# Optimization experiments

Measured on AMD Instinct MI355X. Metric: run time of the kernel, lower is better.

Reference implementation:

```python
import jax, jax.numpy as jnp
import numpy as np

NUM_TAGS = 512
START_TAG = 510
STOP_TAG = 511
BATCH = 128
SEQ_LEN = 512
NEG_INF = -10000.0


def setup_inputs() -> dict:
    key = jax.random.key(0)
    k1, k2, k3 = jax.random.split(key, 3)
    inputs = jax.random.normal(k1, (BATCH, SEQ_LEN, NUM_TAGS), dtype=jnp.float32)
    tags = jax.random.randint(k2, (BATCH, SEQ_LEN), 0, NUM_TAGS)
    transitions = jax.random.normal(k3, (NUM_TAGS, NUM_TAGS), dtype=jnp.float32)
    # match the torch __init__ sentinel masking of the transition matrix
    transitions = transitions.at[START_TAG, :].set(NEG_INF)
    transitions = transitions.at[:, STOP_TAG].set(NEG_INF)
    return {"inputs": inputs, "tags": tags, "transitions": transitions}


def reference(inputs, tags, transitions):
    # inputs: [B, S, T] emission scores; transitions[j, i] = score of i -> j
    B, S, T = inputs.shape
    alpha0 = jnp.full((B, T), NEG_INF, dtype=inputs.dtype)
    alpha0 = alpha0.at[:, START_TAG].set(0.0)

    def step(alpha, emit):
        # alpha: [B, T] (prev tags), emit: [B, T] (next tags)
        # scores[b, next, prev] = alpha[b, prev] + transitions[next, prev]
        scores = alpha[:, None, :] + transitions[None, :, :]  # [B, T, T]
        new_alpha = emit + jax.nn.logsumexp(scores, axis=-1)   # [B, T]
        return new_alpha, None

    emits = jnp.moveaxis(inputs, 1, 0)  # [S, B, T]
    alpha, _ = jax.lax.scan(step, alpha0, emits)

    terminal = alpha + transitions[STOP_TAG][None, :]  # [B, T]
    losses = jax.nn.logsumexp(terminal, axis=-1)       # [B]
    return jnp.sum(losses)
```

## Files before the change

### kernel.cpp

```cpp
#include <hip/hip_runtime.h>
#include <stdint.h>

#define NTAGS 512
#define STAG 510
#define PTAG 511
#define SEQ 512
#define L2E 1.4426950408889634f
#define LN2 0.6931471805599453f
#define MARGIN 13

typedef int   v8i __attribute__((ext_vector_type(8)));
typedef float v4f __attribute__((ext_vector_type(4)));

__device__ __forceinline__ float fexp2(float x) {
#if __has_builtin(__builtin_amdgcn_exp2f)
    return __builtin_amdgcn_exp2f(x);
#else
    float r; asm("v_exp_f32 %0, %1\n\ts_nop 1" : "=v"(r) : "v"(x)); return r;
#endif
}

#define DPPMAX(X, CTRL) fmaxf((X), __int_as_float(__builtin_amdgcn_update_dpp( \
    0, __float_as_int(X), (CTRL), 0xF, 0xF, false)))

#define STEP_SYNC() asm volatile("s_waitcnt lgkmcnt(0)\n\ts_barrier" ::: "memory")

#define WS_SC   196608
#define WS_PART 204800

__global__ void crf_setup_k(const float* __restrict__ trans, uint8_t* __restrict__ ws)
{
    int t = blockIdx.x * blockDim.x + threadIdx.x;
    int n = t >> 4, KB = t & 15;
    const float* row = trans + n * NTAGS;
    int wq = KB >> 1, h = KB & 1;
    float v[32]; float mx = -3.0e38f;
    #pragma unroll
    for (int k = 0; k < 32; ++k) {
        int p = wq*64 + (k & 3)*16 + h*8 + (k >> 2);
        v[k] = row[p]; mx = fmaxf(mx, v[k]);
    }
    int e = (int)floorf(mx * L2E - 2.90689059f);
    int byt = e + 127; byt = byt < 0 ? 0 : (byt > 254 ? 254 : byt);
    float eeff = (float)(byt - 127);
    uint32_t out[6] = {0u,0u,0u,0u,0u,0u};
    #pragma unroll
    for (int k = 0; k < 32; ++k) {
        float q = exp2f(v[k] * L2E - eeff);
        int code;
        if      (q < 2.0f) code = (int)(q * 8.0f + 0.5f);
        else if (q < 4.0f) code = 16 + (int)((q - 2.0f) * 4.0f + 0.5f);
        else               code = 24 + (int)((q - 4.0f) * 2.0f + 0.5f);
        code = code > 31 ? 31 : code;
        int bp = 6*k, d = bp >> 5, off = bp & 31;
        out[d] |= (uint32_t)code << off;
        if (off > 26) out[d+1] |= (uint32_t)code >> (32 - off);
    }
    uint32_t* E6 = (uint32_t*)ws;
    int base = (n*16 + KB) * 6;
    #pragma unroll
    for (int d = 0; d < 6; ++d) E6[base + d] = out[d];
    ws[WS_SC + n*16 + (KB & 3)*4 + (KB >> 2)] = (uint8_t)byt;
}

__global__ __launch_bounds__(512, 2) void crf_main_k(
    const float* __restrict__ inp, const float* __restrict__ trans,
    const uint8_t* __restrict__ ws, float* __restrict__ part)
{
    __shared__ uint8_t aqb[2*8192];
    __shared__ int     mxp[2*16];
    __shared__ float   mxb[16*8];
    __shared__ float   ssum[16*8];
    __shared__ float   Gb[16];

    const int tid = threadIdx.x;
    const int w = tid >> 6, l = tid & 63, c = l & 15, g = l >> 4;
    const int wg = blockIdx.x;
    const int b0 = g * 4;
    const int SCA = 0x78787878;

    v8i Bf[16];
    int esc[4];
    #pragma unroll
    for (int i = 0; i < 4; ++i) {
        const int n = (w*4 + i)*16 + c;
        esc[i] = *(const int*)(ws + WS_SC + n*16 + g*4);
        #pragma unroll
        for (int kk = 0; kk < 4; ++kk) {
            const uint2* p2 = (const uint2*)((const uint32_t*)ws + (n*16 + kk*4 + g)*6);
            uint2 d0 = p2[0], d1 = p2[1], d2 = p2[2];
            v8i bv;
            bv[0]=(int)d0.x; bv[1]=(int)d0.y; bv[2]=(int)d1.x;
            bv[3]=(int)d1.y; bv[4]=(int)d2.x; bv[5]=(int)d2.y;
            bv[6]=0; bv[7]=0;
            Bf[i*4 + kk] = bv;
        }
    }
    #pragma unroll
    for (int i = 0; i < 16; ++i) asm volatile("" : "+v"(Bf[i]));
    #pragma unroll
    for (int i = 0; i < 4; ++i)  asm volatile("" : "+v"(esc[i]));

    const float* ep[4];
    #pragma unroll
    for (int j = 0; j < 4; ++j)
        ep[j] = inp + (size_t)(wg*16 + b0 + j) * (SEQ*NTAGS) + w*64 + c;

    int aqoff[4];
    #pragma unroll
    for (int j = 0; j < 4; ++j) {
        int bb = b0 + j;
        aqoff[j] = bb*128 + (((w*4 + (c>>2)) ^ (bb & 7)) << 2) + (c & 3);
    }

    float vv[4][4];
    {
        float tr[4];
        #pragma unroll
        for (int i = 0; i < 4; ++i) tr[i] = trans[(w*64 + i*16 + c)*NTAGS + STAG];
        #pragma unroll
        for (int j = 0; j < 4; ++j) {
            #pragma unroll
            for (int i = 0; i < 4; ++i)
                vv[j][i] = ep[j][i*16] + tr[i];
        }
    }
    float Mj[4];
    #pragma unroll
    for (int j = 0; j < 4; ++j) {
        float m = fmaxf(fmaxf(vv[j][0], vv[j][1]), fmaxf(vv[j][2], vv[j][3]));
        #pragma unroll
        for (int msk = 1; msk <= 8; msk <<= 1) m = fmaxf(m, __shfl_xor(m, msk, 64));
        if (c == 0) mxb[(b0 + j)*8 + w] = m;
    }
    __syncthreads();
    float G[4];
    #pragma unroll
    for (int j = 0; j < 4; ++j) {
        float m = -3.0e38f;
        #pragma unroll
        for (int k = 0; k < 8; ++k) m = fmaxf(m, mxb[(b0 + j)*8 + k]);
        Mj[j] = m;
        G[j] = m * L2E;
    }
    {
        uint32_t* AQ = (uint32_t*)(aqb + 8192);
        #pragma unroll
        for (int j = 0; j < 4; ++j) {
            float q0 = fexp2((vv[j][0] - Mj[j]) * L2E + 7.0f);
            float q1 = fexp2((vv[j][1] - Mj[j]) * L2E + 7.0f);
            float q2 = fexp2((vv[j][2] - Mj[j]) * L2E + 7.0f);
            float q3 = fexp2((vv[j][3] - Mj[j]) * L2E + 7.0f);
            int t_ = __builtin_amdgcn_cvt_pk_fp8_f32(q0, q1, 0, false);
            t_ = __builtin_amdgcn_cvt_pk_fp8_f32(q2, q3, t_, true);
            AQ[aqoff[j]] = (uint32_t)t_;
        }
    }
    if (w == 0 && c == 0) { int4 z; z.x=0; z.y=0; z.z=0; z.w=0; *(int4*)&mxp[16 + g*4] = z; }

    float emn[4][4];
    #pragma unroll
    for (int j = 0; j < 4; ++j) ep[j] += NTAGS;
    #pragma unroll
    for (int j = 0; j < 4; ++j) {
        #pragma unroll
        for (int i = 0; i < 4; ++i) emn[j][i] = ep[j][i*16];
    }
    __syncthreads();

    int aoffA[8];
    #pragma unroll
    for (int kk = 0; kk < 4; ++kk) {
        aoffA[2*kk]   = c*32 + ((kk*8 + g*2)     ^ (c & 7));
        aoffA[2*kk+1] = c*32 + ((kk*8 + g*2 + 1) ^ (c & 7));
    }

#define MFMA_K(KK) do { \
    v8i A_; \
    *(int4*)&A_       = aq4[aoffA[2*(KK)]]; \
    *(((int4*)&A_)+1) = aq4[aoffA[2*(KK)+1]]; \
    D[0] = __builtin_amdgcn_mfma_scale_f32_16x16x128_f8f6f4(A_, Bf[0*4+(KK)], D[0], 0, 2, (KK), SCA, (KK), esc[0]); \
    D[1] = __builtin_amdgcn_mfma_scale_f32_16x16x128_f8f6f4(A_, Bf[1*4+(KK)], D[1], 0, 2, (KK), SCA, (KK), esc[1]); \
    D[2] = __builtin_amdgcn_mfma_scale_f32_16x16x128_f8f6f4(A_, Bf[2*4+(KK)], D[2], 0, 2, (KK), SCA, (KK), esc[2]); \
    D[3] = __builtin_amdgcn_mfma_scale_f32_16x16x128_f8f6f4(A_, Bf[3*4+(KK)], D[3], 0, 2, (KK), SCA, (KK), esc[3]); \
} while (0)

    for (int s = 1; s < SEQ; ++s) {
        const int cur = s & 1, nxt = cur ^ 1;

        int4 Pv = *(const int4*)&mxp[cur*16 + g*4];
        int Rj[4]; float dmj[4];
        #pragma unroll
        for (int j = 0; j < 4; ++j) {
            Rj[j] = ((const int*)&Pv)[j] + MARGIN;
            dmj[j] = (float)(7 - Rj[j]);
        }

        float emx[4][4];
        #pragma unroll
        for (int j = 0; j < 4; ++j) {
            #pragma unroll
            for (int i = 0; i < 4; ++i)
                emx[j][i] = fexp2(fmaf(emn[j][i], L2E, dmj[j]));
        }
        if (s < SEQ - 1) {
            #pragma unroll
            for (int j = 0; j < 4; ++j) ep[j] += NTAGS;
            #pragma unroll
            for (int j = 0; j < 4; ++j) {
                #pragma unroll
                for (int i = 0; i < 4; ++i) emn[j][i] = ep[j][i*16];
            }
        }

        const int4* aq4 = (const int4*)(aqb + cur*8192);

        v4f D[4];
        #pragma unroll
        for (int i = 0; i < 4; ++i) { D[i][0]=0.f; D[i][1]=0.f; D[i][2]=0.f; D[i][3]=0.f; }
        __builtin_amdgcn_s_setprio(1);
        MFMA_K(0); MFMA_K(1); MFMA_K(2); MFMA_K(3);
        __builtin_amdgcn_s_setprio(0);

        if (s < SEQ - 1) {
            #pragma unroll
            for (int j = 0; j < 4; ++j) G[j] += (float)Rj[j];

            float vq[4][4];
            #pragma unroll
            for (int j = 0; j < 4; ++j) {
                #pragma unroll
                for (int i = 0; i < 4; ++i)
                    vq[j][i] = fminf(D[i][j] * emx[j][i], 448.0f);
            }
            uint32_t* AQ = (uint32_t*)(aqb + nxt*8192);
            #pragma unroll
            for (int j = 0; j < 4; ++j) {
                int t_ = __builtin_amdgcn_cvt_pk_fp8_f32(vq[j][0], vq[j][1], 0, false);
                t_ = __builtin_amdgcn_cvt_pk_fp8_f32(vq[j][2], vq[j][3], t_, true);
                AQ[aqoff[j]] = (uint32_t)t_;
            }
            if (w == 0) {
                int4 post;
                #pragma unroll
                for (int j = 0; j < 4; ++j) {
                    float bm = fmaxf(fmaxf(vq[j][0], vq[j][1]), fmaxf(vq[j][2], vq[j][3]));
                    bm = DPPMAX(bm, 0xB1); bm = DPPMAX(bm, 0x4E);
                    bm = DPPMAX(bm, 0x141); bm = DPPMAX(bm, 0x140);
                    int be = (int)((__float_as_uint(bm) >> 23) & 255u) - 127;
                    be = be < -30 ? -30 : be;
                    ((int*)&post)[j] = be - 7;
                }
                if (c == 0) *(int4*)&mxp[nxt*16 + g*4] = post;
            }
            STEP_SYNC();
        } else {
            float ts[4];
            #pragma unroll
            for (int i = 0; i < 4; ++i) ts[i] = trans[PTAG*NTAGS + w*64 + i*16 + c];
            float x[4][4];
            #pragma unroll
            for (int j = 0; j < 4; ++j) {
                #pragma unroll
                for (int i = 0; i < 4; ++i)
                    x[j][i] = __log2f(D[i][j]) + (emn[j][i] + ts[i]) * L2E;
            }
            #pragma unroll
            for (int j = 0; j < 4; ++j) {
                float m = fmaxf(fmaxf(x[j][0], x[j][1]), fmaxf(x[j][2], x[j][3]));
                #pragma unroll
                for (int msk = 1; msk <= 8; msk <<= 1) m = fmaxf(m, __shfl_xor(m, msk, 64));
                if (c == 0) mxb[(b0 + j)*8 + w] = m;
            }
            if (w == 0 && c == 0) {
                #pragma unroll
                for (int j = 0; j < 4; ++j) Gb[b0 + j] = G[j];
            }
            __syncthreads();
            #pragma unroll
            for (int j = 0; j < 4; ++j) {
                float XM = -3.0e38f;
                #pragma unroll
                for (int k = 0; k < 8; ++k) XM = fmaxf(XM, mxb[(b0 + j)*8 + k]);
                float sj = fexp2(x[j][0] - XM) + fexp2(x[j][1] - XM)
                         + fexp2(x[j][2] - XM) + fexp2(x[j][3] - XM);
                #pragma unroll
                for (int msk = 1; msk <= 8; msk <<= 1) sj += __shfl_xor(sj, msk, 64);
                if (c == 0) ssum[(b0 + j)*8 + w] = sj;
            }
            __syncthreads();
            if (tid < 16) {
                float S = 0.f, XM = -3.0e38f;
                #pragma unroll
                for (int k = 0; k < 8; ++k) { S += ssum[tid*8 + k]; XM = fmaxf(XM, mxb[tid*8 + k]); }
                part[wg*16 + tid] = LN2 * (Gb[tid] + XM + __log2f(S));
            }
        }
    }
#undef MFMA_K
}

__global__ void crf_final_k(const float* __restrict__ part, float* __restrict__ out)
{
    int t = threadIdx.x;
    float vsum = part[t] + part[t + 64];
    #pragma unroll
    for (int off = 32; off; off >>= 1) vsum += __shfl_down(vsum, off, 64);
    if (t == 0) out[0] = vsum;
}

extern "C" void kernel_launch(void* const* d_in, const int* in_sizes, int n_in,
                              void* d_out, int out_size, void* d_ws, size_t ws_size,
                              hipStream_t stream)
{
    (void)in_sizes; (void)n_in; (void)out_size; (void)ws_size;
    const float* inp   = (const float*)d_in[0];
    const float* trans = (const float*)d_in[2];
    uint8_t* ws = (uint8_t*)d_ws;
    float* part = (float*)(ws + WS_PART);

    crf_setup_k<<<64, 128, 0, stream>>>(trans, ws);
    crf_main_k<<<8, 512, 0, stream>>>(inp, trans, ws, part);
    crf_final_k<<<1, 64, 0, stream>>>(part, (float*)d_out);
}
```

Measured before the change: 646.4 us.

## Halve waves per block, give each wave twice the tag columns, hoist A loads

After: 851.8 us. 31.8% more time.

```diff
diff --git a/kernel.cpp b/kernel.cpp
--- a/kernel.cpp
+++ b/kernel.cpp
@@ -33,11 +33,10 @@
     int t = blockIdx.x * blockDim.x + threadIdx.x;
     int n = t >> 4, KB = t & 15;
     const float* row = trans + n * NTAGS;
-    int wq = KB >> 1, h = KB & 1;
     float v[32]; float mx = -3.0e38f;
     #pragma unroll
     for (int k = 0; k < 32; ++k) {
-        int p = wq*64 + (k & 3)*16 + h*8 + (k >> 2);
+        int p = (KB>>2)*128 + (((KB>>1)&1)*4 + (k&3))*16 + (KB&1)*8 + (k>>2);
         v[k] = row[p]; mx = fmaxf(mx, v[k]);
     }
     int e = (int)floorf(mx * L2E - 2.90689059f);
@@ -63,14 +62,14 @@
     ws[WS_SC + n*16 + (KB & 3)*4 + (KB >> 2)] = (uint8_t)byt;
 }
 
-__global__ __launch_bounds__(512, 2) void crf_main_k(
+__global__ __launch_bounds__(256, 1) void crf_main_k(
     const float* __restrict__ inp, const float* __restrict__ trans,
     const uint8_t* __restrict__ ws, float* __restrict__ part)
 {
     __shared__ uint8_t aqb[2*8192];
     __shared__ int     mxp[2*16];
-    __shared__ float   mxb[16*8];
-    __shared__ float   ssum[16*8];
+    __shared__ float   mxb[16*4];
+    __shared__ float   ssum[16*4];
     __shared__ float   Gb[16];
 
     const int tid = threadIdx.x;
@@ -79,11 +78,11 @@
     const int b0 = g * 4;
     const int SCA = 0x78787878;
 
-    v8i Bf[16];
-    int esc[4];
-    #pragma unroll
-    for (int i = 0; i < 4; ++i) {
-        const int n = (w*4 + i)*16 + c;
+    v8i Bf[32];
+    int esc[8];
+    #pragma unroll
+    for (int i = 0; i < 8; ++i) {
+        const int n = (w*8 + i)*16 + c;
         esc[i] = *(const int*)(ws + WS_SC + n*16 + g*4);
         #pragma unroll
         for (int kk = 0; kk < 4; ++kk) {
@@ -97,77 +96,22 @@
         }
     }
     #pragma unroll
-    for (int i = 0; i < 16; ++i) asm volatile("" : "+v"(Bf[i]));
-    #pragma unroll
-    for (int i = 0; i < 4; ++i)  asm volatile("" : "+v"(esc[i]));
+    for (int i = 0; i < 32; ++i) asm volatile("" : "+a"(Bf[i]));
+    #pragma unroll
+    for (int i = 0; i < 8; ++i)  asm volatile("" : "+v"(esc[i]));
 
     const float* ep[4];
     #pragma unroll
     for (int j = 0; j < 4; ++j)
-        ep[j] = inp + (size_t)(wg*16 + b0 + j) * (SEQ*NTAGS) + w*64 + c;
-
-    int aqoff[4];
+        ep[j] = inp + (size_t)(wg*16 + b0 + j) * (SEQ*NTAGS) + w*128 + c;
+
+    int aqoff0[4], aqoff1[4];
     #pragma unroll
     for (int j = 0; j < 4; ++j) {
         int bb = b0 + j;
-        aqoff[j] = bb*128 + (((w*4 + (c>>2)) ^ (bb & 7)) << 2) + (c & 3);
-    }
-
-    float vv[4][4];
-    {
-        float tr[4];
-        #pragma unroll
-        for (int i = 0; i < 4; ++i) tr[i] = trans[(w*64 + i*16 + c)*NTAGS + STAG];
-        #pragma unroll
-        for (int j = 0; j < 4; ++j) {
-            #pragma unroll
-            for (int i = 0; i < 4; ++i)
-                vv[j][i] = ep[j][i*16] + tr[i];
-        }
-    }
-    float Mj[4];
-    #pragma unroll
-    for (int j = 0; j < 4; ++j) {
-        float m = fmaxf(fmaxf(vv[j][0], vv[j][1]), fmaxf(vv[j][2], vv[j][3]));
-        #pragma unroll
-        for (int msk = 1; msk <= 8; msk <<= 1) m = fmaxf(m, __shfl_xor(m, msk, 64));
-        if (c == 0) mxb[(b0 + j)*8 + w] = m;
-    }
-    __syncthreads();
-    float G[4];
-    #pragma unroll
-    for (int j = 0; j < 4; ++j) {
-        float m = -3.0e38f;
-        #pragma unroll
-        for (int k = 0; k < 8; ++k) m = fmaxf(m, mxb[(b0 + j)*8 + k]);
-        Mj[j] = m;
-        G[j] = m * L2E;
-    }
-    {
-        uint32_t* AQ = (uint32_t*)(aqb + 8192);
-        #pragma unroll
-        for (int j = 0; j < 4; ++j) {
-            float q0 = fexp2((vv[j][0] - Mj[j]) * L2E + 7.0f);
-            float q1 = fexp2((vv[j][1] - Mj[j]) * L2E + 7.0f);
-            float q2 = fexp2((vv[j][2] - Mj[j]) * L2E + 7.0f);
-            float q3 = fexp2((vv[j][3] - Mj[j]) * L2E + 7.0f);
-            int t_ = __builtin_amdgcn_cvt_pk_fp8_f32(q0, q1, 0, false);
-            t_ = __builtin_amdgcn_cvt_pk_fp8_f32(q2, q3, t_, true);
-            AQ[aqoff[j]] = (uint32_t)t_;
-        }
-    }
-    if (w == 0 && c == 0) { int4 z; z.x=0; z.y=0; z.z=0; z.w=0; *(int4*)&mxp[16 + g*4] = z; }
-
-    float emn[4][4];
-    #pragma unroll
-    for (int j = 0; j < 4; ++j) ep[j] += NTAGS;
-    #pragma unroll
-    for (int j = 0; j < 4; ++j) {
-        #pragma unroll
-        for (int i = 0; i < 4; ++i) emn[j][i] = ep[j][i*16];
-    }
-    __syncthreads();
-
+        aqoff0[j] = bb*128 + (((w*8 + 0 + (c>>2)) ^ (bb & 7)) << 2) + (c & 3);
+        aqoff1[j] = bb*128 + (((w*8 + 4 + (c>>2)) ^ (bb & 7)) << 2) + (c & 3);
+    }
     int aoffA[8];
     #pragma unroll
     for (int kk = 0; kk < 4; ++kk) {
@@ -175,32 +119,94 @@
         aoffA[2*kk+1] = c*32 + ((kk*8 + g*2 + 1) ^ (c & 7));
     }
 
+    float vv[4][8];
+    {
+        float tr[8];
+        #pragma unroll
+        for (int i = 0; i < 8; ++i) tr[i] = trans[(w*128 + i*16 + c)*NTAGS + STAG];
+        #pragma unroll
+        for (int j = 0; j < 4; ++j) {
+            #pragma unroll
+            for (int i = 0; i < 8; ++i)
+                vv[j][i] = ep[j][i*16] + tr[i];
+        }
+    }
+    float Mj[4];
+    #pragma unroll
+    for (int j = 0; j < 4; ++j) {
+        float m = -3.0e38f;
+        #pragma unroll
+        for (int i = 0; i < 8; ++i) m = fmaxf(m, vv[j][i]);
+        #pragma unroll
+        for (int msk = 1; msk <= 8; msk <<= 1) m = fmaxf(m, __shfl_xor(m, msk, 64));
+        if (c == 0) mxb[(b0 + j)*4 + w] = m;
+    }
+    __syncthreads();
+    float G[4];
+    #pragma unroll
+    for (int j = 0; j < 4; ++j) {
+        float m = -3.0e38f;
+        #pragma unroll
+        for (int k = 0; k < 4; ++k) m = fmaxf(m, mxb[(b0 + j)*4 + k]);
+        Mj[j] = m;
+        G[j] = m * L2E;
+    }
+    {
+        uint32_t* AQ = (uint32_t*)(aqb + 8192);
+        #pragma unroll
+        for (int j = 0; j < 4; ++j) {
+            float q[8];
+            #pragma unroll
+            for (int i = 0; i < 8; ++i) q[i] = fexp2((vv[j][i] - Mj[j]) * L2E + 7.0f);
+            int t0 = __builtin_amdgcn_cvt_pk_fp8_f32(q[0], q[1], 0, false);
+            t0 = __builtin_amdgcn_cvt_pk_fp8_f32(q[2], q[3], t0, true);
+            int t1 = __builtin_amdgcn_cvt_pk_fp8_f32(q[4], q[5], 0, false);
+            t1 = __builtin_amdgcn_cvt_pk_fp8_f32(q[6], q[7], t1, true);
+            AQ[aqoff0[j]] = (uint32_t)t0;
+            AQ[aqoff1[j]] = (uint32_t)t1;
+        }
+    }
+    if (w == 0 && c == 0) { int4 z; z.x=0; z.y=0; z.z=0; z.w=0; *(int4*)&mxp[16 + g*4] = z; }
+
+    float emn[4][8];
+    #pragma unroll
+    for (int j = 0; j < 4; ++j) ep[j] += NTAGS;
+    #pragma unroll
+    for (int j = 0; j < 4; ++j) {
+        #pragma unroll
+        for (int i = 0; i < 8; ++i) emn[j][i] = ep[j][i*16];
+    }
+    __syncthreads();
+
 #define MFMA_K(KK) do { \
     v8i A_; \
-    *(int4*)&A_       = aq4[aoffA[2*(KK)]]; \
-    *(((int4*)&A_)+1) = aq4[aoffA[2*(KK)+1]]; \
-    D[0] = __builtin_amdgcn_mfma_scale_f32_16x16x128_f8f6f4(A_, Bf[0*4+(KK)], D[0], 0, 2, (KK), SCA, (KK), esc[0]); \
-    D[1] = __builtin_amdgcn_mfma_scale_f32_16x16x128_f8f6f4(A_, Bf[1*4+(KK)], D[1], 0, 2, (KK), SCA, (KK), esc[1]); \
-    D[2] = __builtin_amdgcn_mfma_scale_f32_16x16x128_f8f6f4(A_, Bf[2*4+(KK)], D[2], 0, 2, (KK), SCA, (KK), esc[2]); \
-    D[3] = __builtin_amdgcn_mfma_scale_f32_16x16x128_f8f6f4(A_, Bf[3*4+(KK)], D[3], 0, 2, (KK), SCA, (KK), esc[3]); \
+    *(int4*)&A_       = Areg[2*(KK)]; \
+    *(((int4*)&A_)+1) = Areg[2*(KK)+1]; \
+    _Pragma("unroll") \
+    for (int i = 0; i < 8; ++i) \
+        D[i] = __builtin_amdgcn_mfma_scale_f32_16x16x128_f8f6f4(A_, Bf[i*4+(KK)], D[i], 0, 2, (KK), SCA, (KK), esc[i]); \
 } while (0)
 
     for (int s = 1; s < SEQ; ++s) {
         const int cur = s & 1, nxt = cur ^ 1;
 
         int4 Pv = *(const int4*)&mxp[cur*16 + g*4];
+        const int4* aq4 = (const int4*)(aqb + cur*8192);
+        int4 Areg[8];
+        #pragma unroll
+        for (int t = 0; t < 8; ++t) Areg[t] = aq4[aoffA[t]];
+
         int Rj[4]; float dmj[4];
         #pragma unroll
         for (int j = 0; j < 4; ++j) {
             Rj[j] = ((const int*)&Pv)[j] + MARGIN;
             dmj[j] = (float)(7 - Rj[j]);
         }
-
-        float emx[4][4];
+        float emx[4][8];
         #pragma unroll
         for (int j = 0; j < 4; ++j) {
             #pragma unroll
-            for (int i = 0; i < 4; ++i)
+            for (int i = 0; i < 8; ++i)
                 emx[j][i] = fexp2(fmaf(emn[j][i], L2E, dmj[j]));
         }
         if (s < SEQ - 1) {
@@ -209,15 +215,13 @@
             #pragma unroll
             for (int j = 0; j < 4; ++j) {
                 #pragma unroll
-                for (int i = 0; i < 4; ++i) emn[j][i] = ep[j][i*16];
-            }
-        }
-
-        const int4* aq4 = (const int4*)(aqb + cur*8192);
-
-        v4f D[4];
-        #pragma unroll
-        for (int i = 0; i < 4; ++i) { D[i][0]=0.f; D[i][1]=0.f; D[i][2]=0.f; D[i][3]=0.f; }
+                for (int i = 0; i < 8; ++i) emn[j][i] = ep[j][i*16];
+            }
+        }
+
+        v4f D[8];
+        #pragma unroll
+        for (int i = 0; i < 8; ++i) { D[i][0]=0.f; D[i][1]=0.f; D[i][2]=0.f; D[i][3]=0.f; }
         __builtin_amdgcn_s_setprio(1);
         MFMA_K(0); MFMA_K(1); MFMA_K(2); MFMA_K(3);
         __builtin_amdgcn_s_setprio(0);
@@ -226,25 +230,30 @@
             #pragma unroll
             for (int j = 0; j < 4; ++j) G[j] += (float)Rj[j];
 
-            float vq[4][4];
-            #pragma unroll
-            for (int j = 0; j < 4; ++j) {
-                #pragma unroll
-                for (int i = 0; i < 4; ++i)
+            float vq[4][8];
+            #pragma unroll
+            for (int j = 0; j < 4; ++j) {
+                #pragma unroll
+                for (int i = 0; i < 8; ++i)
                     vq[j][i] = fminf(D[i][j] * emx[j][i], 448.0f);
             }
             uint32_t* AQ = (uint32_t*)(aqb + nxt*8192);
             #pragma unroll
             for (int j = 0; j < 4; ++j) {
-                int t_ = __builtin_amdgcn_cvt_pk_fp8_f32(vq[j][0], vq[j][1], 0, false);
-                t_ = __builtin_amdgcn_cvt_pk_fp8_f32(vq[j][2], vq[j][3], t_, true);
-                AQ[aqoff[j]] = (uint32_t)t_;
+                int t0 = __builtin_amdgcn_cvt_pk_fp8_f32(vq[j][0], vq[j][1], 0, false);
+                t0 = __builtin_amdgcn_cvt_pk_fp8_f32(vq[j][2], vq[j][3], t0, true);
+                int t1 = __builtin_amdgcn_cvt_pk_fp8_f32(vq[j][4], vq[j][5], 0, false);
+                t1 = __builtin_amdgcn_cvt_pk_fp8_f32(vq[j][6], vq[j][7], t1, true);
+                AQ[aqoff0[j]] = (uint32_t)t0;
+                AQ[aqoff1[j]] = (uint32_t)t1;
             }
             if (w == 0) {
                 int4 post;
                 #pragma unroll
                 for (int j = 0; j < 4; ++j) {
-                    float bm = fmaxf(fmaxf(vq[j][0], vq[j][1]), fmaxf(vq[j][2], vq[j][3]));
+                    float bm = -3.0e38f;
+                    #pragma unroll
+                    for (int i = 0; i < 8; ++i) bm = fmaxf(bm, vq[j][i]);
                     bm = DPPMAX(bm, 0xB1); bm = DPPMAX(bm, 0x4E);
                     bm = DPPMAX(bm, 0x141); bm = DPPMAX(bm, 0x140);
                     int be = (int)((__float_as_uint(bm) >> 23) & 255u) - 127;
@@ -255,22 +264,24 @@
             }
             STEP_SYNC();
         } else {
-            float ts[4];
-            #pragma unroll
-            for (int i = 0; i < 4; ++i) ts[i] = trans[PTAG*NTAGS + w*64 + i*16 + c];
-            float x[4][4];
-            #pragma unroll
-            for (int j = 0; j < 4; ++j) {
-                #pragma unroll
-                for (int i = 0; i < 4; ++i)
+            float ts[8];
+            #pragma unroll
+            for (int i = 0; i < 8; ++i) ts[i] = trans[PTAG*NTAGS + w*128 + i*16 + c];
+            float x[4][8];
+            #pragma unroll
+            for (int j = 0; j < 4; ++j) {
+                #pragma unroll
+                for (int i = 0; i < 8; ++i)
                     x[j][i] = __log2f(D[i][j]) + (emn[j][i] + ts[i]) * L2E;
             }
             #pragma unroll
             for (int j = 0; j < 4; ++j) {
-                float m = fmaxf(fmaxf(x[j][0], x[j][1]), fmaxf(x[j][2], x[j][3]));
+                float m = -3.0e38f;
+                #pragma unroll
+                for (int i = 0; i < 8; ++i) m = fmaxf(m, x[j][i]);
                 #pragma unroll
                 for (int msk = 1; msk <= 8; msk <<= 1) m = fmaxf(m, __shfl_xor(m, msk, 64));
-                if (c == 0) mxb[(b0 + j)*8 + w] = m;
+                if (c == 0) mxb[(b0 + j)*4 + w] = m;
             }
             if (w == 0 && c == 0) {
                 #pragma unroll
@@ -281,18 +292,19 @@
             for (int j = 0; j < 4; ++j) {
                 float XM = -3.0e38f;
                 #pragma unroll
-                for (int k = 0; k < 8; ++k) XM = fmaxf(XM, mxb[(b0 + j)*8 + k]);
-                float sj = fexp2(x[j][0] - XM) + fexp2(x[j][1] - XM)
-                         + fexp2(x[j][2] - XM) + fexp2(x[j][3] - XM);
+                for (int k = 0; k < 4; ++k) XM = fmaxf(XM, mxb[(b0 + j)*4 + k]);
+                float sj = 0.f;
+                #pragma unroll
+                for (int i = 0; i < 8; ++i) sj += fexp2(x[j][i] - XM);
                 #pragma unroll
                 for (int msk = 1; msk <= 8; msk <<= 1) sj += __shfl_xor(sj, msk, 64);
-                if (c == 0) ssum[(b0 + j)*8 + w] = sj;
+                if (c == 0) ssum[(b0 + j)*4 + w] = sj;
             }
             __syncthreads();
             if (tid < 16) {
                 float S = 0.f, XM = -3.0e38f;
                 #pragma unroll
-                for (int k = 0; k < 8; ++k) { S += ssum[tid*8 + k]; XM = fmaxf(XM, mxb[tid*8 + k]); }
+                for (int k = 0; k < 4; ++k) { S += ssum[tid*4 + k]; XM = fmaxf(XM, mxb[tid*4 + k]); }
                 part[wg*16 + tid] = LN2 * (Gb[tid] + XM + __log2f(S));
             }
         }
@@ -320,6 +332,6 @@
     float* part = (float*)(ws + WS_PART);
 
     crf_setup_k<<<64, 128, 0, stream>>>(trans, ws);
-    crf_main_k<<<8, 512, 0, stream>>>(inp, trans, ws, part);
+    crf_main_k<<<8, 256, 0, stream>>>(inp, trans, ws, part);
     crf_final_k<<<1, 64, 0, stream>>>(part, (float*)d_out);
 }
```
